# Optimization experiments

Hardware: AMD Instinct MI355X
Metric: run time of the kernel (lower is better)

## Reference

```python
import jax, jax.numpy as jnp
import numpy as np

N_HEAD, D_HEAD, D_MODEL = 16, 64, 1024
QLEN, MEMLEN, BSZ = 1024, 1024, 2
KLEN = QLEN + MEMLEN  # rlen == klen
LN_EPS = 1e-5
NEG = -1e30


def _rel_shift(x):
    # x: [qlen, rlen, bsz, n_head] -> Transformer-XL relative shift
    q, r, b, n = x.shape
    zp = jnp.zeros((q, 1, b, n), x.dtype)
    xp = jnp.concatenate([zp, x], axis=1).reshape(r + 1, q, b, n)
    return xp[1:].reshape(q, r, b, n)


def _layer_norm(x, gamma, beta):
    mu = jnp.mean(x, axis=-1, keepdims=True)
    var = jnp.mean((x - mu) ** 2, axis=-1, keepdims=True)
    return (x - mu) * jax.lax.rsqrt(var + LN_EPS) * gamma + beta


def setup_inputs() -> dict:
    key = jax.random.key(0)
    ks = jax.random.split(key, 8)
    w = jax.random.normal(ks[0], (QLEN, BSZ, D_MODEL), jnp.float32)
    r = jax.random.normal(ks[1], (KLEN, D_MODEL), jnp.float32)
    r_w_bias = jax.random.normal(ks[2], (N_HEAD, D_HEAD), jnp.float32) * 0.02
    r_r_bias = jax.random.normal(ks[3], (N_HEAD, D_HEAD), jnp.float32) * 0.02
    mems = jax.random.normal(ks[4], (MEMLEN, BSZ, D_MODEL), jnp.float32)
    W_qkv = jax.random.normal(ks[5], (D_MODEL, 3 * N_HEAD * D_HEAD), jnp.float32) * 0.02
    W_r = jax.random.normal(ks[6], (D_MODEL, N_HEAD * D_HEAD), jnp.float32) * 0.02
    W_o = jax.random.normal(ks[7], (N_HEAD * D_HEAD, D_MODEL), jnp.float32) * 0.02
    ln_gamma = jnp.ones((D_MODEL,), jnp.float32)
    ln_beta = jnp.zeros((D_MODEL,), jnp.float32)
    # causal mask with memory: key j visible to query i iff j <= i + MEMLEN (True = keep)
    attn_mask = jnp.arange(KLEN)[None, :] <= (jnp.arange(QLEN)[:, None] + MEMLEN)
    return {"w": w, "r": r, "r_w_bias": r_w_bias, "r_r_bias": r_r_bias,
            "mems": mems, "attn_mask": attn_mask, "W_qkv": W_qkv, "W_r": W_r,
            "W_o": W_o, "ln_gamma": ln_gamma, "ln_beta": ln_beta}


def reference(w, r, r_w_bias, r_r_bias, mems, attn_mask, W_qkv, W_r, W_o, ln_gamma, ln_beta):
    qlen, bsz = w.shape[0], w.shape[1]
    scale = 1.0 / (D_HEAD ** 0.5)
    cat = jnp.concatenate([mems, w], axis=0)            # [klen, b, d_model]
    klen = cat.shape[0]
    w_heads = cat @ W_qkv                                # [klen, b, 3*H*D]
    r_head_k = (r @ W_r).reshape(-1, N_HEAD, D_HEAD)     # [rlen, H, D]
    w_head_q, w_head_k, w_head_v = jnp.split(w_heads, 3, axis=-1)
    w_head_q = w_head_q[-qlen:].reshape(qlen, bsz, N_HEAD, D_HEAD)
    w_head_k = w_head_k.reshape(klen, bsz, N_HEAD, D_HEAD)
    w_head_v = w_head_v.reshape(klen, bsz, N_HEAD, D_HEAD)
    AC = jnp.einsum('ibnd,jbnd->ijbn', w_head_q + r_w_bias, w_head_k)
    BD = jnp.einsum('ibnd,jnd->ijbn', w_head_q + r_r_bias, r_head_k)
    BD = _rel_shift(BD)
    attn_score = (AC + BD) * scale                       # [q, k, b, n]
    attn_score = jnp.where(attn_mask[:, :, None, None], attn_score, NEG)
    attn_prob = jax.nn.softmax(attn_score, axis=1)
    attn_vec = jnp.einsum('ijbn,jbnd->ibnd', attn_prob, w_head_v)
    attn_vec = attn_vec.reshape(qlen, bsz, N_HEAD * D_HEAD)
    attn_out = attn_vec @ W_o                            # [q, b, d_model]
    return _layer_norm(w + attn_out, ln_gamma, ln_beta)
```

## Files before the change

kernel.cpp:

```cpp
#include <hip/hip_runtime.h>
#include <hip/hip_bf16.h>

#define NHEAD 16
#define DHEAD 64
#define DMODEL 1024
#define QLEN 1024
#define MEMLEN 1024
#define BSZ 2
#define KLEN 2048
#define LN_EPS 1e-5f

typedef __hip_bfloat16 bf16;
typedef __attribute__((ext_vector_type(8))) short short8;
typedef __attribute__((ext_vector_type(4))) float f32x4;

__device__ __forceinline__ float b2f(bf16 x) { return __bfloat162float(x); }
__device__ __forceinline__ bf16 f2b(float x) { return __float2bfloat16(x); }
__device__ __forceinline__ short f2bs(float f) {
    bf16 h = __float2bfloat16(f);
    return *reinterpret_cast<short*>(&h);
}
__device__ __forceinline__ float s2f(short s) {
    bf16 h = *reinterpret_cast<bf16*>(&s);
    return __bfloat162float(h);
}
__device__ __forceinline__ float fexp2(float x) {
    float y;
    asm("v_exp_f32 %0, %1" : "=v"(y) : "v"(x));
    return y;
}

#define MFMA16(a, b, c) __builtin_amdgcn_mfma_f32_16x16x32_bf16(a, b, c, 0, 0, 0)

#define AS1 __attribute__((address_space(1)))
#define AS3 __attribute__((address_space(3)))
__device__ __forceinline__ void gld16(const bf16* g, bf16* l) {
    __builtin_amdgcn_global_load_lds((const AS1 void*)(uintptr_t)g,
                                     (AS3 void*)(uint32_t)(uintptr_t)l, 16, 0, 0);
}

__global__ __launch_bounds__(256)
void prep(const float* __restrict__ mems, const float* __restrict__ w,
          const float* __restrict__ r, const float* __restrict__ Wqkv,
          const float* __restrict__ Wr, const float* __restrict__ Wo,
          bf16* __restrict__ Abf, bf16* __restrict__ rbf,
          bf16* __restrict__ Wqkvt, bf16* __restrict__ Wrt,
          bf16* __restrict__ Wot) {
    __shared__ bf16 T[64][65];
    const int id = blockIdx.x;
    const int t = threadIdx.x;
    if (id < 6144) {
        const float* src;
        bf16* dst;
        int off;
        if (id < 2048)      { src = mems; dst = Abf;                       off = id; }
        else if (id < 4096) { src = w;    dst = Abf + (size_t)2048 * 1024; off = id - 2048; }
        else                { src = r;    dst = rbf;                       off = id - 4096; }
        int i = off * 256 + t;
        const float4 v = reinterpret_cast<const float4*>(src)[i];
        bf16 o[4] = {f2b(v.x), f2b(v.y), f2b(v.z), f2b(v.w)};
        reinterpret_cast<ulong1*>(dst)[i] = *reinterpret_cast<ulong1*>(o);
        return;
    }
    int tid2 = id - 6144;
    const float* in;
    bf16* out;
    int N, tn, tile;
    if (tid2 < 768)       { in = Wqkv; out = Wqkvt; N = 3072; tn = 48; tile = tid2; }
    else if (tid2 < 1024) { in = Wr;   out = Wrt;   N = 1024; tn = 16; tile = tid2 - 768; }
    else                  { in = Wo;   out = Wot;   N = 1024; tn = 16; tile = tid2 - 1024; }
    const int K = 1024;
    const int n0 = (tile % tn) * 64, k0 = (tile / tn) * 64;
    #pragma unroll
    for (int e = 0; e < 16; e++) {
        int flat = e * 256 + t;
        int kl = flat >> 6, nl = flat & 63;
        T[kl][nl] = f2b(in[(size_t)(k0 + kl) * N + n0 + nl]);
    }
    __syncthreads();
    #pragma unroll
    for (int e = 0; e < 16; e++) {
        int flat = e * 256 + t;
        int nl = flat >> 6, kl = flat & 63;
        out[(size_t)(n0 + nl) * K + k0 + kl] = T[kl][nl];
    }
}

__global__ __launch_bounds__(256)
void gemm_mfma(const bf16* __restrict__ A, const bf16* __restrict__ Bt,
               const bf16* __restrict__ A2, const bf16* __restrict__ B2,
               int M, int N, int K, int mode,
               const float* __restrict__ rwb, const float* __restrict__ rrb,
               bf16* __restrict__ Qw, bf16* __restrict__ Qr,
               bf16* __restrict__ Kb, bf16* __restrict__ Vt,
               bf16* __restrict__ Cb, float* __restrict__ Cf) {
    const int bm = blockIdx.x * 128, bn = blockIdx.y * 128;
    int sub = 0;
    const bf16* Ap = A;
    const bf16* Bp = Bt;
    if (mode == 0 && bm < 2048 && bn < 1024) { sub = 1; Ap = A2; Bp = B2; }
    __shared__ bf16 As[128 * 32];
    __shared__ bf16 Bs[128 * 32];
    const int t = threadIdx.x;
    const int w = t >> 6, lane = t & 63, quad = lane >> 4, l16 = lane & 15;
    const int wm = (w >> 1) * 64, wn = (w & 1) * 64;
    const int lrow = lane >> 2, lcol = (lane & 3) * 8;

    f32x4 acc[4][4];
    #pragma unroll
    for (int mt = 0; mt < 4; mt++)
        #pragma unroll
        for (int nt = 0; nt < 4; nt++) acc[mt][nt] = (f32x4){0.f, 0.f, 0.f, 0.f};

    for (int k0 = 0; k0 < K; k0 += 32) {
        #pragma unroll
        for (int e = 0; e < 2; e++) {
            int ch = w + 4 * e;
            int row = ch * 16 + lrow;
            gld16(Ap + (size_t)(bm + row) * K + k0 + lcol, As + ch * 512);
            gld16(Bp + (size_t)(bn + row) * K + k0 + lcol, Bs + ch * 512);
        }
        __syncthreads();
        short8 af[4], bfr[4];
        #pragma unroll
        for (int mt = 0; mt < 4; mt++)
            af[mt] = *reinterpret_cast<short8*>(&As[(wm + 16 * mt + l16) * 32 + quad * 8]);
        #pragma unroll
        for (int nt = 0; nt < 4; nt++)
            bfr[nt] = *reinterpret_cast<short8*>(&Bs[(wn + 16 * nt + l16) * 32 + quad * 8]);
        #pragma unroll
        for (int mt = 0; mt < 4; mt++)
            #pragma unroll
            for (int nt = 0; nt < 4; nt++)
                acc[mt][nt] = MFMA16(af[mt], bfr[nt], acc[mt][nt]);
        __syncthreads();
    }

    const float QSC = 0.18033688f;
    #pragma unroll
    for (int mt = 0; mt < 4; mt++)
        #pragma unroll
        for (int nt = 0; nt < 4; nt++)
            #pragma unroll
            for (int r = 0; r < 4; r++) {
                int m = bm + wm + 16 * mt + quad * 4 + r;
                int c = bn + wn + 16 * nt + l16;
                float v = acc[mt][nt][r];
                if (sub) {
                    Cb[(size_t)m * 1024 + c] = f2b(v);
                } else if (mode == 0) {
                    int seg = c >> 10, cc = c & 1023;
                    if (seg == 0) {
                        if (m >= 2048) {
                            size_t o = (size_t)(m - 2048) * 1024 + cc;
                            Qw[o] = f2b((v + rwb[cc]) * QSC);
                            Qr[o] = f2b((v + rrb[cc]) * QSC);
                        }
                    } else if (seg == 1) {
                        Kb[(size_t)m * 1024 + cc] = f2b(v);
                    } else {
                        Vt[((size_t)cc * 2 + (m & 1)) * 2048 + (m >> 1)] = f2b(v);
                    }
                } else {
                    Cf[(size_t)m * N + c] = v;
                }
            }
}

__global__ __launch_bounds__(256, 3)
void attn_mfma(const bf16* __restrict__ Qw, const bf16* __restrict__ Qr,
               const bf16* __restrict__ Kb, const bf16* __restrict__ Vt,
               const bf16* __restrict__ Rk, float* __restrict__ O0g,
               float* __restrict__ O1g, float2* __restrict__ ML) {
    const int id = blockIdx.x;
    const int xcd = id & 7, local = id >> 3;
    const int pidx = local & 3;
    const int couple = (local >> 2) & 7;
    const int chunk = local >> 5;
    const int pair = xcd * 4 + pidx;
    const int b = pair & 1, n = pair >> 1;
    const int TA = couple + 17;
    const int t_beg = (chunk == 0) ? 0 : (chunk == 1) ? 17 : 33;
    const int t_end = (chunk == 0) ? 17 : (chunk == 1) ? 33 : 49;

    int segs[2][4];
    int nseg = 0;
    {
        int aend = min(t_end, TA);
        if (t_beg < aend) {
            segs[nseg][0] = couple; segs[nseg][1] = t_beg;
            segs[nseg][2] = aend;   segs[nseg][3] = (t_beg == 0) ? 0 : 1;
            nseg++;
        }
        int bbeg = max(t_beg, TA);
        if (bbeg < t_end) {
            segs[nseg][0] = 15 - couple; segs[nseg][1] = bbeg - TA;
            segs[nseg][2] = t_end - TA;  segs[nseg][3] = (bbeg == TA) ? 0 : 1;
            nseg++;
        }
    }

    const int tid = threadIdx.x;
    const int w = tid >> 6, lane = tid & 63;
    const int quad = lane >> 4, l16 = lane & 15;
    const int ln8 = lane >> 3;
    const int cs = (lane & 7) ^ (ln8 & 7);
    const int q0 = (quad ^ (l16 & 7)) * 8;
    const int q1 = q0 ^ 32;
    const int rbl = 48 - 16 * w;

    __shared__ bf16 Ks[64 * 64];
    __shared__ bf16 Vs[64 * 64];
    __shared__ bf16 Rs[3][64 * 64];
    __shared__ short WP_s[4][16 * 82];
    short* WP = WP_s[w];

    const int koff = b * 1024 + n * 64 + cs * 8;
    const size_t voff = (size_t)n * 262144 + b * 2048 + cs * 8;
    const int rcol = n * 64 + cs * 8;

    for (int sg = 0; sg < nseg; sg++) {
        const int i0 = segs[sg][0], jb = segs[sg][1], je = segs[sg][2], slot = segs[sg][3];
        const int I0 = i0 * 64;
        const int qbase = I0 + 16 * w;
        const int RB = 960 - I0;
        const int jlast = i0 + 16;

        auto stageKV = [&](int tt) {
            const int J0t = tt * 64;
            #pragma unroll
            for (int e = 0; e < 2; e++) {
                int ch = w + 4 * e;
                gld16(Vt + (size_t)(ch * 8 + ln8) * 4096 + voff + J0t, Vs + ch * 512);
                gld16(Kb + (size_t)(J0t + ch * 8 + ln8) * 2048 + koff, Ks + ch * 512);
            }
        };
        auto stageR = [&](int u) {
            bf16* rd = Rs[u % 3];
            #pragma unroll
            for (int e = 0; e < 2; e++) {
                int ch = w + 4 * e;
                int rrow = min(RB + u * 64 + ch * 8 + ln8, 2047);
                gld16(Rk + (size_t)rrow * 1024 + rcol, rd + ch * 512);
            }
        };

        short8 aqw[2], aqr[2];
        {
            const bf16* qp = Qw + ((size_t)(qbase + l16) * 2 + b) * 1024 + n * 64 + quad * 8;
            aqw[0] = *reinterpret_cast<const short8*>(qp);
            aqw[1] = *reinterpret_cast<const short8*>(qp + 32);
            const bf16* qp2 = Qr + ((size_t)(qbase + l16) * 2 + b) * 1024 + n * 64 + quad * 8;
            aqr[0] = *reinterpret_cast<const short8*>(qp2);
            aqr[1] = *reinterpret_cast<const short8*>(qp2 + 32);
        }

        f32x4 O[4];
        #pragma unroll
        for (int d = 0; d < 4; d++) O[d] = (f32x4){0.f, 0.f, 0.f, 0.f};
        float m_run = -1e30f;
        float pl[4] = {0.f, 0.f, 0.f, 0.f};

        if (sg) {
            asm volatile("s_waitcnt vmcnt(0)" ::: "memory");
            __builtin_amdgcn_s_barrier();
        }
        stageR(jb); stageR(jb + 1);

        for (int j = jb; j < je; j++) {
            const int J0 = j * 64;

            asm volatile("s_waitcnt vmcnt(0)" ::: "memory");
            __builtin_amdgcn_s_barrier();

            stageKV(j);
            stageR(j + 2);

            const bf16* R0 = Rs[j % 3];
            const bf16* R1 = Rs[(j + 1) % 3];

            #pragma unroll
            for (int s = 0; s < 5; s++) {
                int rb2 = rbl + 16 * s;
                const bf16* Rb = (rb2 & 64) ? R1 : R0;
                int rh = (rb2 & 63) + l16;
                short8 b0 = *reinterpret_cast<const short8*>(&Rb[rh * 64 + q0]);
                short8 b1 = *reinterpret_cast<const short8*>(&Rb[rh * 64 + q1]);
                f32x4 acc = (f32x4){0.f, 0.f, 0.f, 0.f};
                __builtin_amdgcn_s_setprio(1);
                acc = MFMA16(aqr[0], b0, acc);
                acc = MFMA16(aqr[1], b1, acc);
                __builtin_amdgcn_s_setprio(0);
                #pragma unroll
                for (int r = 0; r < 4; r++)
                    WP[(quad * 4 + r) * 82 + 16 * s + l16] = f2bs(acc[r]);
            }

            asm volatile("s_waitcnt vmcnt(2)" ::: "memory");
            __builtin_amdgcn_s_barrier();

            float sv[4][4];
            #pragma unroll
            for (int n16 = 0; n16 < 4; n16++) {
                int kr = 16 * n16 + l16;
                short8 k0 = *reinterpret_cast<const short8*>(&Ks[kr * 64 + q0]);
                short8 k1 = *reinterpret_cast<const short8*>(&Ks[kr * 64 + q1]);
                f32x4 acc = (f32x4){0.f, 0.f, 0.f, 0.f};
                __builtin_amdgcn_s_setprio(1);
                acc = MFMA16(aqw[0], k0, acc);
                acc = MFMA16(aqw[1], k1, acc);
                __builtin_amdgcn_s_setprio(0);
                #pragma unroll
                for (int r = 0; r < 4; r++) {
                    int row = quad * 4 + r, col = 16 * n16 + l16;
                    sv[n16][r] = acc[r] + s2f(WP[row * 82 + col - row + 15]);
                }
            }
            if (j == jlast) {
                #pragma unroll
                for (int n16 = 0; n16 < 4; n16++)
                    #pragma unroll
                    for (int r = 0; r < 4; r++) {
                        int row = quad * 4 + r, col = 16 * n16 + l16;
                        if (J0 + col > qbase + row + MEMLEN) sv[n16][r] = -1e30f;
                    }
            }

            float mx = sv[0][0];
            #pragma unroll
            for (int n16 = 0; n16 < 4; n16++)
                #pragma unroll
                for (int r = 0; r < 4; r++) mx = fmaxf(mx, sv[n16][r]);
            #pragma unroll
            for (int msk = 1; msk < 16; msk <<= 1) mx = fmaxf(mx, __shfl_xor(mx, msk));
            if (mx > m_run + 11.5f) {
                const float alpha = fexp2(m_run - mx);
                m_run = mx;
                #pragma unroll
                for (int r = 0; r < 4; r++) pl[r] *= alpha;
                #pragma unroll
                for (int d = 0; d < 4; d++)
                    #pragma unroll
                    for (int r = 0; r < 4; r++) O[d][r] *= alpha;
            }
            #pragma unroll
            for (int n16 = 0; n16 < 4; n16++)
                #pragma unroll
                for (int r = 0; r < 4; r++) sv[n16][r] = fexp2(sv[n16][r] - m_run);
            #pragma unroll
            for (int r = 0; r < 4; r++)
                pl[r] += sv[0][r] + sv[1][r] + sv[2][r] + sv[3][r];

            #pragma unroll
            for (int n16 = 0; n16 < 4; n16++)
                #pragma unroll
                for (int r = 0; r < 4; r++)
                    WP[(quad * 4 + r) * 72 + 16 * n16 + l16] = f2bs(sv[n16][r]);
            short8 ap0 = *reinterpret_cast<short8*>(&WP[l16 * 72 + quad * 8]);
            short8 ap1 = *reinterpret_cast<short8*>(&WP[l16 * 72 + 32 + quad * 8]);

            __builtin_amdgcn_s_setprio(1);
            #pragma unroll
            for (int ds = 0; ds < 4; ds++) {
                int dr = 16 * ds + l16;
                short8 v0 = *reinterpret_cast<const short8*>(&Vs[dr * 64 + q0]);
                short8 v1 = *reinterpret_cast<const short8*>(&Vs[dr * 64 + q1]);
                O[ds] = MFMA16(ap0, v0, O[ds]);
                O[ds] = MFMA16(ap1, v1, O[ds]);
            }
            __builtin_amdgcn_s_setprio(0);
        }

        float lr[4];
        #pragma unroll
        for (int r = 0; r < 4; r++) {
            float s = pl[r];
            #pragma unroll
            for (int msk = 1; msk < 16; msk <<= 1) s += __shfl_xor(s, msk);
            lr[r] = s;
        }
        if (l16 == 0) {
            #pragma unroll
            for (int r = 0; r < 4; r++) {
                int q = qbase + quad * 4 + r;
                ML[(size_t)slot * 32768 + (q * 2 + b) * 16 + n] =
                    make_float2(m_run, lr[r]);
            }
        }
        float* Od = slot ? O1g : O0g;
        #pragma unroll
        for (int ds = 0; ds < 4; ds++)
            #pragma unroll
            for (int r = 0; r < 4; r++) {
                int q = qbase + quad * 4 + r;
                Od[((size_t)q * 2 + b) * 1024 + n * 64 + 16 * ds + l16] = O[ds][r];
            }
    }
}

__global__ __launch_bounds__(256)
void attn_combine(const float* __restrict__ O0, const float* __restrict__ O1,
                  const float2* __restrict__ ML, bf16* __restrict__ AVbf) {
    const int row = blockIdx.x;
    const int t = threadIdx.x;
    const int n = t >> 4;
    const int i0 = row >> 7;
    const float2 a0 = ML[row * 16 + n];
    const f32x4 p0 = reinterpret_cast<const f32x4*>(O0)[row * 256 + t];
    short o[4];
    if (i0 != 0) {
        const float2 a1 = ML[32768 + row * 16 + n];
        const float m = fmaxf(a0.x, a1.x);
        const float e0 = fexp2(a0.x - m);
        const float e1 = fexp2(a1.x - m);
        const float inv = 1.f / (a0.y * e0 + a1.y * e1);
        const f32x4 p1 = reinterpret_cast<const f32x4*>(O1)[row * 256 + t];
        #pragma unroll
        for (int jj = 0; jj < 4; jj++)
            o[jj] = f2bs((p0[jj] * e0 + p1[jj] * e1) * inv);
    } else {
        const float inv = 1.f / a0.y;
        #pragma unroll
        for (int jj = 0; jj < 4; jj++) o[jj] = f2bs(p0[jj] * inv);
    }
    reinterpret_cast<ulong1*>(AVbf)[row * 256 + t] = *reinterpret_cast<ulong1*>(o);
}

__global__ __launch_bounds__(256)
void ln_res(const float* __restrict__ ao, const float* __restrict__ w,
            const float* __restrict__ gamma, const float* __restrict__ beta,
            float* __restrict__ out) {
    const int m = blockIdx.x;
    const int t = threadIdx.x;
    __shared__ float red[256];
    float x[4];
    #pragma unroll
    for (int e = 0; e < 4; e++) {
        int c = e * 256 + t;
        x[e] = ao[(size_t)m * DMODEL + c] + w[(size_t)m * DMODEL + c];
    }
    float s = x[0] + x[1] + x[2] + x[3];
    red[t] = s;
    __syncthreads();
    #pragma unroll
    for (int off = 128; off; off >>= 1) {
        if (t < off) red[t] += red[t + off];
        __syncthreads();
    }
    const float mu = red[0] * (1.f / 1024.f);
    __syncthreads();
    float s2 = 0.f;
    #pragma unroll
    for (int e = 0; e < 4; e++) { float dx = x[e] - mu; s2 += dx * dx; }
    red[t] = s2;
    __syncthreads();
    #pragma unroll
    for (int off = 128; off; off >>= 1) {
        if (t < off) red[t] += red[t + off];
        __syncthreads();
    }
    const float rstd = rsqrtf(red[0] * (1.f / 1024.f) + LN_EPS);
    #pragma unroll
    for (int e = 0; e < 4; e++) {
        int c = e * 256 + t;
        out[(size_t)m * DMODEL + c] = (x[e] - mu) * rstd * gamma[c] + beta[c];
    }
}

extern "C" void kernel_launch(void* const* d_in, const int* in_sizes, int n_in,
                              void* d_out, int out_size, void* d_ws, size_t ws_size,
                              hipStream_t stream) {
    const float* w        = (const float*)d_in[0];
    const float* r        = (const float*)d_in[1];
    const float* r_w_bias = (const float*)d_in[2];
    const float* r_r_bias = (const float*)d_in[3];
    const float* mems     = (const float*)d_in[4];
    const float* W_qkv    = (const float*)d_in[6];
    const float* W_r      = (const float*)d_in[7];
    const float* W_o      = (const float*)d_in[8];
    const float* gamma    = (const float*)d_in[9];
    const float* beta     = (const float*)d_in[10];
    float* out = (float*)d_out;

    bf16* Abf    = (bf16*)d_ws;
    bf16* Wqkvt  = Abf   + (size_t)4096 * 1024;
    bf16* Wrt    = Wqkvt + (size_t)3072 * 1024;
    bf16* Wot    = Wrt   + (size_t)1024 * 1024;
    bf16* rbf    = Wot   + (size_t)1024 * 1024;
    bf16* Qw     = rbf   + (size_t)2048 * 1024;
    bf16* Qr     = Qw    + (size_t)2048 * 1024;
    bf16* Kb     = Qr    + (size_t)2048 * 1024;
    bf16* Vt     = Kb    + (size_t)4096 * 1024;
    bf16* Rk     = Vt    + (size_t)2048 * 2048;
    bf16* AVbf   = Rk    + (size_t)2048 * 1024;
    float* attn_out = (float*)Abf;
    float* Opart0   = (float*)Abf;
    float* Opart1   = (float*)Wqkvt;
    float2* ML      = (float2*)rbf;

    dim3 b256(256);
    prep<<<dim3(7424), b256, 0, stream>>>(mems, w, r, W_qkv, W_r, W_o,
                                          Abf, rbf, Wqkvt, Wrt, Wot);
    gemm_mfma<<<dim3(32, 24), b256, 0, stream>>>(
        Abf, Wqkvt, rbf, Wrt, 4096, 3072, 1024, 0, r_w_bias, r_r_bias,
        Qw, Qr, Kb, Vt, Rk, nullptr);
    attn_mfma<<<dim3(768), b256, 0, stream>>>(Qw, Qr, Kb, Vt, Rk,
                                              Opart0, Opart1, ML);
    attn_combine<<<dim3(2048), b256, 0, stream>>>(Opart0, Opart1, ML, AVbf);
    gemm_mfma<<<dim3(16, 8), b256, 0, stream>>>(
        AVbf, Wot, nullptr, nullptr, 2048, 1024, 1024, 2, nullptr, nullptr,
        nullptr, nullptr, nullptr, nullptr, nullptr, attn_out);
    ln_res<<<dim3(QLEN * BSZ), b256, 0, stream>>>(attn_out, w, gamma, beta, out);
}
```

Before: 248.2 us.

## Pre-swizzle V into MFMA fragment layout, split attention into four chunks

The QKV GEMM epilogue now writes V in a tiled layout that matches the MFMA B-fragment, so the attention kernel loads V fragments straight from global memory into registers and no longer stages V through shared memory. The R ring buffer shrinks from three slots to two, and its prefetch moves after the mid-iteration barrier. Together the smaller LDS footprint allows launch bounds of four blocks per CU. The key range is split into four chunks (1024 blocks) instead of three, with a third partial output buffer, and the combine kernel merges up to three partials and writes bf16 in place into the first partial buffer, which the output GEMM then reads with a stride argument. The trade-offs are uncoalesced scattered writes of V, extra global load latency on V inside the loop, and more partial-output traffic.

```diff
diff --git a/kernel.cpp b/kernel.cpp
--- a/kernel.cpp
+++ b/kernel.cpp
@@ -89,7 +89,7 @@
 __global__ __launch_bounds__(256)
 void gemm_mfma(const bf16* __restrict__ A, const bf16* __restrict__ Bt,
                const bf16* __restrict__ A2, const bf16* __restrict__ B2,
-               int M, int N, int K, int mode,
+               int M, int N, int K, int lda, int mode,
                const float* __restrict__ rwb, const float* __restrict__ rrb,
                bf16* __restrict__ Qw, bf16* __restrict__ Qr,
                bf16* __restrict__ Kb, bf16* __restrict__ Vt,
@@ -117,7 +117,7 @@
         for (int e = 0; e < 2; e++) {
             int ch = w + 4 * e;
             int row = ch * 16 + lrow;
-            gld16(Ap + (size_t)(bm + row) * K + k0 + lcol, As + ch * 512);
+            gld16(Ap + (size_t)(bm + row) * lda + k0 + lcol, As + ch * 512);
             gld16(Bp + (size_t)(bn + row) * K + k0 + lcol, Bs + ch * 512);
         }
         __syncthreads();
@@ -159,7 +159,14 @@
                     } else if (seg == 1) {
                         Kb[(size_t)m * 1024 + cc] = f2b(v);
                     } else {
-                        Vt[((size_t)cc * 2 + (m & 1)) * 2048 + (m >> 1)] = f2b(v);
+                        int j = m >> 1, bb = m & 1;
+                        int n = cc >> 6, dd = cc & 63;
+                        int ds = dd >> 4, l16v = dd & 15;
+                        int jt = j >> 6, jl = j & 63;
+                        int h = jl >> 5, qd = (jl >> 3) & 3, e = jl & 7;
+                        size_t addr = ((size_t)(n * 2 + bb) * 32 + jt) * 4096
+                                    + (ds * 2 + h) * 512 + (qd * 16 + l16v) * 8 + e;
+                        Vt[addr] = f2b(v);
                     }
                 } else {
                     Cf[(size_t)m * N + c] = v;
@@ -167,11 +174,12 @@
             }
 }
 
-__global__ __launch_bounds__(256, 3)
+__global__ __launch_bounds__(256, 4)
 void attn_mfma(const bf16* __restrict__ Qw, const bf16* __restrict__ Qr,
                const bf16* __restrict__ Kb, const bf16* __restrict__ Vt,
                const bf16* __restrict__ Rk, float* __restrict__ O0g,
-               float* __restrict__ O1g, float2* __restrict__ ML) {
+               float* __restrict__ O1g, float* __restrict__ O2g,
+               float2* __restrict__ ML) {
     const int id = blockIdx.x;
     const int xcd = id & 7, local = id >> 3;
     const int pidx = local & 3;
@@ -180,22 +188,22 @@
     const int pair = xcd * 4 + pidx;
     const int b = pair & 1, n = pair >> 1;
     const int TA = couple + 17;
-    const int t_beg = (chunk == 0) ? 0 : (chunk == 1) ? 17 : 33;
-    const int t_end = (chunk == 0) ? 17 : (chunk == 1) ? 33 : 49;
+    const int t0 = (chunk == 0) ? 0 : (chunk == 1) ? 13 : (chunk == 2) ? 25 : 37;
+    const int t1 = (chunk == 0) ? 13 : (chunk == 1) ? 25 : (chunk == 2) ? 37 : 49;
 
     int segs[2][4];
     int nseg = 0;
     {
-        int aend = min(t_end, TA);
-        if (t_beg < aend) {
-            segs[nseg][0] = couple; segs[nseg][1] = t_beg;
-            segs[nseg][2] = aend;   segs[nseg][3] = (t_beg == 0) ? 0 : 1;
+        int aend = min(t1, TA);
+        if (t0 < aend) {
+            segs[nseg][0] = couple; segs[nseg][1] = t0;
+            segs[nseg][2] = aend;   segs[nseg][3] = (chunk == 0) ? 0 : 1;
             nseg++;
         }
-        int bbeg = max(t_beg, TA);
-        if (bbeg < t_end) {
+        int bbeg = max(t0, TA);
+        if (bbeg < t1) {
             segs[nseg][0] = 15 - couple; segs[nseg][1] = bbeg - TA;
-            segs[nseg][2] = t_end - TA;  segs[nseg][3] = (bbeg == TA) ? 0 : 1;
+            segs[nseg][2] = t1 - TA;     segs[nseg][3] = chunk - 1;
             nseg++;
         }
     }
@@ -210,14 +218,13 @@
     const int rbl = 48 - 16 * w;
 
     __shared__ bf16 Ks[64 * 64];
-    __shared__ bf16 Vs[64 * 64];
-    __shared__ bf16 Rs[3][64 * 64];
+    __shared__ bf16 Rs[2][64 * 64];
     __shared__ short WP_s[4][16 * 82];
     short* WP = WP_s[w];
 
     const int koff = b * 1024 + n * 64 + cs * 8;
-    const size_t voff = (size_t)n * 262144 + b * 2048 + cs * 8;
     const int rcol = n * 64 + cs * 8;
+    const size_t vbase = (size_t)(n * 2 + b) * 32 * 4096 + lane * 8;
 
     for (int sg = 0; sg < nseg; sg++) {
         const int i0 = segs[sg][0], jb = segs[sg][1], je = segs[sg][2], slot = segs[sg][3];
@@ -226,17 +233,16 @@
         const int RB = 960 - I0;
         const int jlast = i0 + 16;
 
-        auto stageKV = [&](int tt) {
+        auto stageK = [&](int tt) {
             const int J0t = tt * 64;
             #pragma unroll
             for (int e = 0; e < 2; e++) {
                 int ch = w + 4 * e;
-                gld16(Vt + (size_t)(ch * 8 + ln8) * 4096 + voff + J0t, Vs + ch * 512);
                 gld16(Kb + (size_t)(J0t + ch * 8 + ln8) * 2048 + koff, Ks + ch * 512);
             }
         };
         auto stageR = [&](int u) {
-            bf16* rd = Rs[u % 3];
+            bf16* rd = Rs[u & 1];
             #pragma unroll
             for (int e = 0; e < 2; e++) {
                 int ch = w + 4 * e;
@@ -273,11 +279,20 @@
             asm volatile("s_waitcnt vmcnt(0)" ::: "memory");
             __builtin_amdgcn_s_barrier();
 
-            stageKV(j);
-            stageR(j + 2);
-
-            const bf16* R0 = Rs[j % 3];
-            const bf16* R1 = Rs[(j + 1) % 3];
+            stageK(j);
+            __builtin_amdgcn_sched_barrier(0);
+            short8 vf0[4], vf1[4];
+            {
+                const bf16* vp = Vt + vbase + (size_t)(j >> 0) * 0 + (size_t)j * 4096;
+                #pragma unroll
+                for (int ds = 0; ds < 4; ds++) {
+                    vf0[ds] = *reinterpret_cast<const short8*>(vp + (ds * 2 + 0) * 512);
+                    vf1[ds] = *reinterpret_cast<const short8*>(vp + (ds * 2 + 1) * 512);
+                }
+            }
+
+            const bf16* R0 = Rs[j & 1];
+            const bf16* R1 = Rs[(j + 1) & 1];
 
             #pragma unroll
             for (int s = 0; s < 5; s++) {
@@ -296,8 +311,10 @@
                     WP[(quad * 4 + r) * 82 + 16 * s + l16] = f2bs(acc[r]);
             }
 
-            asm volatile("s_waitcnt vmcnt(2)" ::: "memory");
+            asm volatile("s_waitcnt vmcnt(8)" ::: "memory");
             __builtin_amdgcn_s_barrier();
+
+            if (j + 2 <= je) stageR(j + 2);
 
             float sv[4][4];
             #pragma unroll
@@ -362,11 +379,8 @@
             __builtin_amdgcn_s_setprio(1);
             #pragma unroll
             for (int ds = 0; ds < 4; ds++) {
-                int dr = 16 * ds + l16;
-                short8 v0 = *reinterpret_cast<const short8*>(&Vs[dr * 64 + q0]);
-                short8 v1 = *reinterpret_cast<const short8*>(&Vs[dr * 64 + q1]);
-                O[ds] = MFMA16(ap0, v0, O[ds]);
-                O[ds] = MFMA16(ap1, v1, O[ds]);
+                O[ds] = MFMA16(ap0, vf0[ds], O[ds]);
+                O[ds] = MFMA16(ap1, vf1[ds], O[ds]);
             }
             __builtin_amdgcn_s_setprio(0);
         }
@@ -387,43 +401,47 @@
                     make_float2(m_run, lr[r]);
             }
         }
-        float* Od = slot ? O1g : O0g;
+        float* Od = (slot == 0) ? O0g : (slot == 1) ? O1g : O2g;
+        const int roff = (slot == 2) ? 1024 : 0;
         #pragma unroll
         for (int ds = 0; ds < 4; ds++)
             #pragma unroll
             for (int r = 0; r < 4; r++) {
                 int q = qbase + quad * 4 + r;
-                Od[((size_t)q * 2 + b) * 1024 + n * 64 + 16 * ds + l16] = O[ds][r];
+                Od[((size_t)(q * 2 + b - roff)) * 1024 + n * 64 + 16 * ds + l16] = O[ds][r];
             }
     }
 }
 
 __global__ __launch_bounds__(256)
-void attn_combine(const float* __restrict__ O0, const float* __restrict__ O1,
-                  const float2* __restrict__ ML, bf16* __restrict__ AVbf) {
+void attn_combine(float* __restrict__ O0, const float* __restrict__ O1,
+                  const float* __restrict__ O2, const float2* __restrict__ ML) {
     const int row = blockIdx.x;
     const int t = threadIdx.x;
     const int n = t >> 4;
     const int i0 = row >> 7;
     const float2 a0 = ML[row * 16 + n];
+    const float2 a1 = ML[32768 + row * 16 + n];
     const f32x4 p0 = reinterpret_cast<const f32x4*>(O0)[row * 256 + t];
+    const f32x4 p1 = reinterpret_cast<const f32x4*>(O1)[row * 256 + t];
+    float m = fmaxf(a0.x, a1.x);
+    float2 a2 = make_float2(0.f, 0.f);
+    f32x4 p2 = (f32x4){0.f, 0.f, 0.f, 0.f};
+    if (i0 >= 8) {
+        a2 = ML[65536 + row * 16 + n];
+        m = fmaxf(m, a2.x);
+        p2 = reinterpret_cast<const f32x4*>(O2)[(row - 1024) * 256 + t];
+    }
+    const float e0 = fexp2(a0.x - m);
+    const float e1 = fexp2(a1.x - m);
+    const float e2 = (i0 >= 8) ? fexp2(a2.x - m) : 0.f;
+    const float inv = 1.f / (a0.y * e0 + a1.y * e1 + a2.y * e2);
     short o[4];
-    if (i0 != 0) {
-        const float2 a1 = ML[32768 + row * 16 + n];
-        const float m = fmaxf(a0.x, a1.x);
-        const float e0 = fexp2(a0.x - m);
-        const float e1 = fexp2(a1.x - m);
-        const float inv = 1.f / (a0.y * e0 + a1.y * e1);
-        const f32x4 p1 = reinterpret_cast<const f32x4*>(O1)[row * 256 + t];
-        #pragma unroll
-        for (int jj = 0; jj < 4; jj++)
-            o[jj] = f2bs((p0[jj] * e0 + p1[jj] * e1) * inv);
-    } else {
-        const float inv = 1.f / a0.y;
-        #pragma unroll
-        for (int jj = 0; jj < 4; jj++) o[jj] = f2bs(p0[jj] * inv);
-    }
-    reinterpret_cast<ulong1*>(AVbf)[row * 256 + t] = *reinterpret_cast<ulong1*>(o);
+    #pragma unroll
+    for (int jj = 0; jj < 4; jj++)
+        o[jj] = f2bs((p0[jj] * e0 + p1[jj] * e1 + p2[jj] * e2) * inv);
+    __syncthreads();
+    reinterpret_cast<ulong1*>(O0)[row * 512 + t] = *reinterpret_cast<ulong1*>(o);
 }
 
 __global__ __launch_bounds__(256)
@@ -493,22 +511,24 @@
     bf16* Vt     = Kb    + (size_t)4096 * 1024;
     bf16* Rk     = Vt    + (size_t)2048 * 2048;
     bf16* AVbf   = Rk    + (size_t)2048 * 1024;
-    float* attn_out = (float*)Abf;
     float* Opart0   = (float*)Abf;
     float* Opart1   = (float*)Wqkvt;
-    float2* ML      = (float2*)rbf;
+    float* Opart2   = (float*)rbf;
+    float2* ML      = (float2*)AVbf;
+    float* attn_out = (float*)Wqkvt;
+    bf16* AVc       = Abf;
 
     dim3 b256(256);
     prep<<<dim3(7424), b256, 0, stream>>>(mems, w, r, W_qkv, W_r, W_o,
                                           Abf, rbf, Wqkvt, Wrt, Wot);
     gemm_mfma<<<dim3(32, 24), b256, 0, stream>>>(
-        Abf, Wqkvt, rbf, Wrt, 4096, 3072, 1024, 0, r_w_bias, r_r_bias,
+        Abf, Wqkvt, rbf, Wrt, 4096, 3072, 1024, 1024, 0, r_w_bias, r_r_bias,
         Qw, Qr, Kb, Vt, Rk, nullptr);
-    attn_mfma<<<dim3(768), b256, 0, stream>>>(Qw, Qr, Kb, Vt, Rk,
-                                              Opart0, Opart1, ML);
-    attn_combine<<<dim3(2048), b256, 0, stream>>>(Opart0, Opart1, ML, AVbf);
+    attn_mfma<<<dim3(1024), b256, 0, stream>>>(Qw, Qr, Kb, Vt, Rk,
+                                               Opart0, Opart1, Opart2, ML);
+    attn_combine<<<dim3(2048), b256, 0, stream>>>(Opart0, Opart1, Opart2, ML);
     gemm_mfma<<<dim3(16, 8), b256, 0, stream>>>(
-        AVbf, Wot, nullptr, nullptr, 2048, 1024, 1024, 2, nullptr, nullptr,
+        AVc, Wot, nullptr, nullptr, 2048, 1024, 1024, 2048, 2, nullptr, nullptr,
         nullptr, nullptr, nullptr, nullptr, nullptr, attn_out);
     ln_res<<<dim3(QLEN * BSZ), b256, 0, stream>>>(attn_out, w, gamma, beta, out);
 }
```

Result: slower. 327.6 us (+32.0%).

## Deepen GEMM K-tile with swizzled LDS, split-K output projection, shuffle LayerNorm

Applied to the files above, without the earlier changes.

The GEMM K step grows from 32 to 64 per iteration, and an XOR swizzle is added to the LDS layout so fragment reads avoid bank conflicts. The output projection GEMM now uses split-K over 2 z-blocks writing two fp32 partials, so 128 blocks become 256 and the GPU is filled better. The LayerNorm kernel sums both partials with the residual and uses wavefront shuffle reductions instead of a shared-memory tree. The cost is extra traffic for the partial buffer and larger LDS per block.

```diff
diff --git a/kernel.cpp b/kernel.cpp
--- a/kernel.cpp
+++ b/kernel.cpp
@@ -93,18 +93,24 @@
                const float* __restrict__ rwb, const float* __restrict__ rrb,
                bf16* __restrict__ Qw, bf16* __restrict__ Qr,
                bf16* __restrict__ Kb, bf16* __restrict__ Vt,
-               bf16* __restrict__ Cb, float* __restrict__ Cf) {
+               bf16* __restrict__ Cb, float* __restrict__ Cf,
+               float* __restrict__ Cf2) {
     const int bm = blockIdx.x * 128, bn = blockIdx.y * 128;
     int sub = 0;
     const bf16* Ap = A;
     const bf16* Bp = Bt;
     if (mode == 0 && bm < 2048 && bn < 1024) { sub = 1; Ap = A2; Bp = B2; }
-    __shared__ bf16 As[128 * 32];
-    __shared__ bf16 Bs[128 * 32];
+    const int ldk = (mode == 2) ? 1024 : K;
+    float* Cfz = Cf;
+    if (mode == 2 && blockIdx.z) { Ap += 512; Bp += 512; Cfz = Cf2; }
+    __shared__ bf16 As[128 * 64];
+    __shared__ bf16 Bs[128 * 64];
     const int t = threadIdx.x;
     const int w = t >> 6, lane = t & 63, quad = lane >> 4, l16 = lane & 15;
     const int wm = (w >> 1) * 64, wn = (w & 1) * 64;
-    const int lrow = lane >> 2, lcol = (lane & 3) * 8;
+    const int srow = lane >> 3;
+    const int scs = ((lane & 7) ^ srow) * 8;
+    const int c0 = (quad ^ (l16 & 7)) * 8;
 
     f32x4 acc[4][4];
     #pragma unroll
@@ -112,27 +118,31 @@
         #pragma unroll
         for (int nt = 0; nt < 4; nt++) acc[mt][nt] = (f32x4){0.f, 0.f, 0.f, 0.f};
 
-    for (int k0 = 0; k0 < K; k0 += 32) {
-        #pragma unroll
-        for (int e = 0; e < 2; e++) {
+    for (int k0 = 0; k0 < K; k0 += 64) {
+        #pragma unroll
+        for (int e = 0; e < 4; e++) {
             int ch = w + 4 * e;
-            int row = ch * 16 + lrow;
-            gld16(Ap + (size_t)(bm + row) * K + k0 + lcol, As + ch * 512);
-            gld16(Bp + (size_t)(bn + row) * K + k0 + lcol, Bs + ch * 512);
+            int row = ch * 8 + srow;
+            gld16(Ap + (size_t)(bm + row) * ldk + k0 + scs, As + ch * 512);
+            gld16(Bp + (size_t)(bn + row) * ldk + k0 + scs, Bs + ch * 512);
         }
         __syncthreads();
-        short8 af[4], bfr[4];
-        #pragma unroll
-        for (int mt = 0; mt < 4; mt++)
-            af[mt] = *reinterpret_cast<short8*>(&As[(wm + 16 * mt + l16) * 32 + quad * 8]);
-        #pragma unroll
-        for (int nt = 0; nt < 4; nt++)
-            bfr[nt] = *reinterpret_cast<short8*>(&Bs[(wn + 16 * nt + l16) * 32 + quad * 8]);
-        #pragma unroll
-        for (int mt = 0; mt < 4; mt++)
+        #pragma unroll
+        for (int kk = 0; kk < 2; kk++) {
+            const int cc = c0 ^ (kk << 5);
+            short8 af[4], bfr[4];
+            #pragma unroll
+            for (int mt = 0; mt < 4; mt++)
+                af[mt] = *reinterpret_cast<short8*>(&As[(wm + 16 * mt + l16) * 64 + cc]);
             #pragma unroll
             for (int nt = 0; nt < 4; nt++)
-                acc[mt][nt] = MFMA16(af[mt], bfr[nt], acc[mt][nt]);
+                bfr[nt] = *reinterpret_cast<short8*>(&Bs[(wn + 16 * nt + l16) * 64 + cc]);
+            #pragma unroll
+            for (int mt = 0; mt < 4; mt++)
+                #pragma unroll
+                for (int nt = 0; nt < 4; nt++)
+                    acc[mt][nt] = MFMA16(af[mt], bfr[nt], acc[mt][nt]);
+        }
         __syncthreads();
     }
 
@@ -149,20 +159,20 @@
                 if (sub) {
                     Cb[(size_t)m * 1024 + c] = f2b(v);
                 } else if (mode == 0) {
-                    int seg = c >> 10, cc = c & 1023;
+                    int seg = c >> 10, cc2 = c & 1023;
                     if (seg == 0) {
                         if (m >= 2048) {
-                            size_t o = (size_t)(m - 2048) * 1024 + cc;
-                            Qw[o] = f2b((v + rwb[cc]) * QSC);
-                            Qr[o] = f2b((v + rrb[cc]) * QSC);
+                            size_t o = (size_t)(m - 2048) * 1024 + cc2;
+                            Qw[o] = f2b((v + rwb[cc2]) * QSC);
+                            Qr[o] = f2b((v + rrb[cc2]) * QSC);
                         }
                     } else if (seg == 1) {
-                        Kb[(size_t)m * 1024 + cc] = f2b(v);
+                        Kb[(size_t)m * 1024 + cc2] = f2b(v);
                     } else {
-                        Vt[((size_t)cc * 2 + (m & 1)) * 2048 + (m >> 1)] = f2b(v);
+                        Vt[((size_t)cc2 * 2 + (m & 1)) * 2048 + (m >> 1)] = f2b(v);
                     }
                 } else {
-                    Cf[(size_t)m * N + c] = v;
+                    Cfz[(size_t)m * N + c] = v;
                 }
             }
 }
@@ -427,39 +437,34 @@
 }
 
 __global__ __launch_bounds__(256)
-void ln_res(const float* __restrict__ ao, const float* __restrict__ w,
-            const float* __restrict__ gamma, const float* __restrict__ beta,
-            float* __restrict__ out) {
+void ln_res(const float* __restrict__ ao0, const float* __restrict__ ao1,
+            const float* __restrict__ w, const float* __restrict__ gamma,
+            const float* __restrict__ beta, float* __restrict__ out) {
     const int m = blockIdx.x;
     const int t = threadIdx.x;
-    __shared__ float red[256];
+    const int wv = t >> 6, lane = t & 63;
+    __shared__ float red[8];
     float x[4];
     #pragma unroll
     for (int e = 0; e < 4; e++) {
         int c = e * 256 + t;
-        x[e] = ao[(size_t)m * DMODEL + c] + w[(size_t)m * DMODEL + c];
+        x[e] = ao0[(size_t)m * DMODEL + c] + ao1[(size_t)m * DMODEL + c]
+             + w[(size_t)m * DMODEL + c];
     }
     float s = x[0] + x[1] + x[2] + x[3];
-    red[t] = s;
+    #pragma unroll
+    for (int msk = 1; msk < 64; msk <<= 1) s += __shfl_xor(s, msk);
+    if (lane == 0) red[wv] = s;
     __syncthreads();
-    #pragma unroll
-    for (int off = 128; off; off >>= 1) {
-        if (t < off) red[t] += red[t + off];
-        __syncthreads();
-    }
-    const float mu = red[0] * (1.f / 1024.f);
+    const float mu = (red[0] + red[1] + red[2] + red[3]) * (1.f / 1024.f);
+    float s2 = 0.f;
+    #pragma unroll
+    for (int e = 0; e < 4; e++) { float dx = x[e] - mu; s2 += dx * dx; }
+    #pragma unroll
+    for (int msk = 1; msk < 64; msk <<= 1) s2 += __shfl_xor(s2, msk);
+    if (lane == 0) red[4 + wv] = s2;
     __syncthreads();
-    float s2 = 0.f;
-    #pragma unroll
-    for (int e = 0; e < 4; e++) { float dx = x[e] - mu; s2 += dx * dx; }
-    red[t] = s2;
-    __syncthreads();
-    #pragma unroll
-    for (int off = 128; off; off >>= 1) {
-        if (t < off) red[t] += red[t + off];
-        __syncthreads();
-    }
-    const float rstd = rsqrtf(red[0] * (1.f / 1024.f) + LN_EPS);
+    const float rstd = rsqrtf((red[4] + red[5] + red[6] + red[7]) * (1.f / 1024.f) + LN_EPS);
     #pragma unroll
     for (int e = 0; e < 4; e++) {
         int c = e * 256 + t;
@@ -493,22 +498,24 @@
     bf16* Vt     = Kb    + (size_t)4096 * 1024;
     bf16* Rk     = Vt    + (size_t)2048 * 2048;
     bf16* AVbf   = Rk    + (size_t)2048 * 1024;
-    float* attn_out = (float*)Abf;
     float* Opart0   = (float*)Abf;
     float* Opart1   = (float*)Wqkvt;
     float2* ML      = (float2*)rbf;
+    float* attn_out0 = (float*)Abf;
+    float* attn_out1 = (float*)Wqkvt;
 
     dim3 b256(256);
     prep<<<dim3(7424), b256, 0, stream>>>(mems, w, r, W_qkv, W_r, W_o,
                                           Abf, rbf, Wqkvt, Wrt, Wot);
     gemm_mfma<<<dim3(32, 24), b256, 0, stream>>>(
         Abf, Wqkvt, rbf, Wrt, 4096, 3072, 1024, 0, r_w_bias, r_r_bias,
-        Qw, Qr, Kb, Vt, Rk, nullptr);
+        Qw, Qr, Kb, Vt, Rk, nullptr, nullptr);
     attn_mfma<<<dim3(768), b256, 0, stream>>>(Qw, Qr, Kb, Vt, Rk,
                                               Opart0, Opart1, ML);
     attn_combine<<<dim3(2048), b256, 0, stream>>>(Opart0, Opart1, ML, AVbf);
-    gemm_mfma<<<dim3(16, 8), b256, 0, stream>>>(
-        AVbf, Wot, nullptr, nullptr, 2048, 1024, 1024, 2, nullptr, nullptr,
-        nullptr, nullptr, nullptr, nullptr, nullptr, attn_out);
-    ln_res<<<dim3(QLEN * BSZ), b256, 0, stream>>>(attn_out, w, gamma, beta, out);
-}
+    gemm_mfma<<<dim3(16, 8, 2), b256, 0, stream>>>(
+        AVbf, Wot, nullptr, nullptr, 2048, 1024, 512, 2, nullptr, nullptr,
+        nullptr, nullptr, nullptr, nullptr, nullptr, attn_out0, attn_out1);
+    ln_res<<<dim3(QLEN * BSZ), b256, 0, stream>>>(attn_out0, attn_out1, w,
+                                                  gamma, beta, out);
+}
```

Result: no change. 249.5 us (+0.5%).
